# Performance work log

Measured on AMD Instinct MI355X. Metric: run time of the kernel, lower is better.

The kernel has to match this reference:

```python
import jax, jax.numpy as jnp
import numpy as np

N_NODES = 50000
N_EDGES = 800000
F_IN = 128
HID = 128
N_GRAPHS = 256


def setup_inputs() -> dict:
    key = jax.random.key(0)
    ks = jax.random.split(key, 12)
    gx = jax.random.normal(ks[0], (N_NODES, F_IN), dtype=jnp.float32)
    edge_index = jax.random.randint(ks[1], (2, N_EDGES), 0, N_NODES, dtype=jnp.int64)
    batch = jnp.sort(jax.random.randint(ks[2], (N_NODES,), 0, N_GRAPHS, dtype=jnp.int64))
    edge_attr = jax.random.uniform(ks[3], (N_EDGES,), dtype=jnp.float32)
    s1 = 1.0 / np.sqrt(F_IN)
    s2 = 1.0 / np.sqrt(HID)
    W1 = jax.random.uniform(ks[4], (F_IN, HID), jnp.float32, -s1, s1)
    b1 = jnp.zeros((HID,), jnp.float32)
    W2 = jax.random.uniform(ks[5], (HID, HID), jnp.float32, -s2, s2)
    b2 = jnp.zeros((HID,), jnp.float32)
    W3 = jax.random.uniform(ks[6], (HID, HID), jnp.float32, -s2, s2)
    b3 = jnp.zeros((HID,), jnp.float32)
    return {"gx": gx, "edge_index": edge_index, "batch": batch, "edge_attr": edge_attr,
            "W1": W1, "b1": b1, "W2": W2, "b2": b2, "W3": W3, "b3": b3}


def _gcn_conv(x, W, b, row, col, edge_weight, n_nodes):
    # PyG GCNConv with add_self_loops=False:
    #   deg[i] = sum of edge_weight over edges with dst == i
    #   norm_e = deg^{-1/2}[row] * w_e * deg^{-1/2}[col]
    #   out[i] = sum_{e: col_e == i} norm_e * (x @ W)[row_e] + b
    deg = jax.ops.segment_sum(edge_weight, col, num_segments=n_nodes)
    dinv = jnp.where(deg > 0, jax.lax.rsqrt(deg), 0.0)
    norm = dinv[row] * edge_weight * dinv[col]  # [E]
    h = x @ W  # [N, H]
    msg = h[row] * norm[:, None]  # [E, H] gather + scale
    out = jax.ops.segment_sum(msg, col, num_segments=n_nodes)  # scatter-add
    return out + b


def reference(gx, edge_index, batch, edge_attr, W1, b1, W2, b2, W3, b3):
    row, col = edge_index[0], edge_index[1]
    n = gx.shape[0]
    # dropout layers are in eval mode (identity) for a deterministic reference
    h = jax.nn.relu(_gcn_conv(gx, W1, b1, row, col, edge_attr, n))
    h = jax.nn.relu(_gcn_conv(h, W2, b2, row, col, edge_attr, n))
    h = _gcn_conv(h, W3, b3, row, col, edge_attr, n)
    readout = jax.ops.segment_sum(h, batch, num_segments=N_GRAPHS)  # global_add_pool
    return h, readout
```

## Files before the change

kernel.cpp:

```cpp
#include <hip/hip_runtime.h>

#define FEAT 128

typedef __attribute__((ext_vector_type(8))) short short8;
typedef __attribute__((ext_vector_type(4))) float f32x4;

__device__ __forceinline__ unsigned int bf16rtn(float f) {
    unsigned int u = __float_as_uint(f);
    return (u + 0x7fffu + ((u >> 16) & 1u)) >> 16;
}
__device__ __forceinline__ float bf16tof(unsigned int h) { return __uint_as_float(h << 16); }
__device__ __forceinline__ float bf16lo(unsigned int v) { return __uint_as_float(v << 16); }
__device__ __forceinline__ float bf16hi(unsigned int v) { return __uint_as_float(v & 0xffff0000u); }

__global__ void zero_kernel(float* __restrict__ p, int n) {
    int i = blockIdx.x * blockDim.x + threadIdx.x;
    if (i < n) p[i] = 0.0f;
}

__global__ __launch_bounds__(256) void hist_kernel(const int* __restrict__ col,
                                                   int* __restrict__ ghist,
                                                   int E, int nblk, int nbuck) {
    __shared__ int h[256];
    const int t = threadIdx.x, b = blockIdx.x;
    h[t] = 0;
    __syncthreads();
    const int base = b * 4096;
#pragma unroll
    for (int i = 0; i < 16; ++i) {
        int e = base + i * 256 + t;
        if (e < E) atomicAdd(&h[col[e] >> 8], 1);
    }
    __syncthreads();
    if (t < nbuck) ghist[t * nblk + b] = h[t];
}

__global__ __launch_bounds__(256) void scan_block_kernel(const int* __restrict__ cnt,
                                                         int* __restrict__ out,
                                                         int* __restrict__ bsum, int M) {
    __shared__ int s[256];
    int t = threadIdx.x;
    int i = blockIdx.x * 256 + t;
    int own = (i < M) ? cnt[i] : 0;
    s[t] = own;
    for (int off = 1; off < 256; off <<= 1) {
        __syncthreads();
        int v = (t >= off) ? s[t - off] : 0;
        __syncthreads();
        s[t] += v;
    }
    __syncthreads();
    if (i < M) out[i] = s[t] - own;
    if (t == 255) bsum[blockIdx.x] = s[255];
}

__global__ __launch_bounds__(256) void scan_bsum_kernel(int* __restrict__ bsum, int nb) {
    __shared__ int s[256];
    int t = threadIdx.x;
    int own = (t < nb) ? bsum[t] : 0;
    s[t] = own;
    for (int off = 1; off < 256; off <<= 1) {
        __syncthreads();
        int v = (t >= off) ? s[t - off] : 0;
        __syncthreads();
        s[t] += v;
    }
    __syncthreads();
    if (t < nb) bsum[t] = s[t] - own;
}

__global__ __launch_bounds__(256) void scatter1_kernel(const int* __restrict__ row,
                                                       const int* __restrict__ col,
                                                       const float* __restrict__ ew,
                                                       const int* __restrict__ gsc,
                                                       const int* __restrict__ bsum,
                                                       uint2* __restrict__ bedge,
                                                       int E, int nblk, int nbuck) {
    __shared__ int cur[256];
    const int t = threadIdx.x, b = blockIdx.x;
    if (t < nbuck) {
        int idx = t * nblk + b;
        cur[t] = gsc[idx] + bsum[idx >> 8];
    }
    __syncthreads();
    const int base = b * 4096;
#pragma unroll
    for (int i = 0; i < 16; ++i) {
        int e = base + i * 256 + t;
        if (e < E) {
            int c = col[e];
            int slot = atomicAdd(&cur[c >> 8], 1);
            bedge[slot] = make_uint2(((unsigned)c << 16) | (unsigned)row[e],
                                     __float_as_uint(ew[e]));
        }
    }
}

__global__ __launch_bounds__(256) void bucket_kernel(const uint2* __restrict__ bedge,
                                                     const int* __restrict__ gsc,
                                                     const int* __restrict__ bsum,
                                                     int* __restrict__ rowptr,
                                                     float* __restrict__ dinv,
                                                     uint2* __restrict__ sedge,
                                                     int N, int E, int nblk, int nbuck) {
    __shared__ int lcnt[256];
    __shared__ float lw[256];
    __shared__ int lscan[256];
    __shared__ int lcur[256];
    __shared__ float ldv[256];

    const int d = blockIdx.x, t = threadIdx.x;
    const int i0 = d * nblk;
    const int base = gsc[i0] + bsum[i0 >> 8];
    int end;
    if (d == nbuck - 1) end = E;
    else {
        const int i1 = (d + 1) * nblk;
        end = gsc[i1] + bsum[i1 >> 8];
    }

    lcnt[t] = 0;
    lw[t] = 0.f;
    __syncthreads();
    for (int i = base + t; i < end; i += 256) {
        uint2 p = bedge[i];
        int c = (p.x >> 16) & 255;
        atomicAdd(&lcnt[c], 1);
        atomicAdd(&lw[c], __uint_as_float(p.y));
    }
    __syncthreads();
    int own = lcnt[t];
    lscan[t] = own;
    for (int off = 1; off < 256; off <<= 1) {
        __syncthreads();
        int v = (t >= off) ? lscan[t - off] : 0;
        __syncthreads();
        lscan[t] += v;
    }
    __syncthreads();
    int excl = lscan[t] - own;
    lcur[t] = base + excl;
    float wsum = lw[t];
    float dv = (wsum > 0.f) ? rsqrtf(wsum) : 0.f;
    ldv[t] = dv;
    int node = d * 256 + t;
    if (node < N) {
        rowptr[node] = base + excl;
        dinv[node] = dv;
    }
    if (d == nbuck - 1 && t == 0) rowptr[N] = E;
    __syncthreads();
    for (int i = base + t; i < end; i += 256) {
        uint2 p = bedge[i];
        int c = (p.x >> 16) & 255;
        int slot = atomicAdd(&lcur[c], 1);
        sedge[slot] = make_uint2(p.x & 0xFFFFu,
                                 __float_as_uint(__uint_as_float(p.y) * ldv[c]));
    }
}

__global__ void norm_kernel(uint2* __restrict__ sedge, const float* __restrict__ dinv, int E) {
    int i = blockIdx.x * blockDim.x + threadIdx.x;
    if (i < E) {
        uint2 p = sedge[i];
        p.y = __float_as_uint(__uint_as_float(p.y) * dinv[p.x]);
        sedge[i] = p;
    }
}

__global__ void convw_kernel(const float* __restrict__ W0, const float* __restrict__ W1,
                             const float* __restrict__ W2,
                             unsigned short* __restrict__ Whi, unsigned short* __restrict__ Wlo) {
    int i = blockIdx.x * blockDim.x + threadIdx.x;
    int which = blockIdx.y;
    const float* W = (which == 0) ? W0 : (which == 1) ? W1 : W2;
    int c = i >> 7, k = i & 127;
    float w = W[(size_t)k * FEAT + c];
    unsigned int h = bf16rtn(w);
    size_t off = (size_t)which * 16384 + (size_t)c * FEAT + k;
    Whi[off] = (unsigned short)h;
    Wlo[off] = (unsigned short)bf16rtn(w - bf16tof(h));
}

__global__ __launch_bounds__(256) void gemm_mfma_kernel(
    const float* __restrict__ X,
    const unsigned short* __restrict__ Wthi, const unsigned short* __restrict__ Wtlo,
    unsigned int* __restrict__ hb,
    int N)
{
    __shared__ unsigned short xh[64 * 128];
    __shared__ unsigned short xl[64 * 128];
    __shared__ unsigned short wh[64 * 128];
    __shared__ unsigned short wl[64 * 128];

    const int tid = threadIdx.x;
    const int r0 = blockIdx.x * 64;
    const int cb = blockIdx.y;

#pragma unroll
    for (int it = 0; it < 4; ++it) {
        int idx = it * 256 + tid;
        int c = idx >> 4;
        int k8 = (idx & 15) * 8;
        int sw = k8 ^ ((c & 7) << 3);
        size_t src = (size_t)(cb * 64 + c) * FEAT + k8;
        *(short8*)&wh[c * 128 + sw] = *(const short8*)(Wthi + src);
        *(short8*)&wl[c * 128 + sw] = *(const short8*)(Wtlo + src);
    }
#pragma unroll
    for (int it = 0; it < 8; ++it) {
        int idx = it * 256 + tid;
        int r = idx >> 5;
        int kc = (idx & 31) * 4;
        int gr = r0 + r;
        float4 v = make_float4(0.f, 0.f, 0.f, 0.f);
        if (gr < N) v = *(const float4*)(X + (size_t)gr * FEAT + kc);
        unsigned int h0 = bf16rtn(v.x), h1 = bf16rtn(v.y);
        unsigned int h2 = bf16rtn(v.z), h3 = bf16rtn(v.w);
        ushort4 hv = make_ushort4((unsigned short)h0, (unsigned short)h1,
                                  (unsigned short)h2, (unsigned short)h3);
        ushort4 lv = make_ushort4((unsigned short)bf16rtn(v.x - bf16tof(h0)),
                                  (unsigned short)bf16rtn(v.y - bf16tof(h1)),
                                  (unsigned short)bf16rtn(v.z - bf16tof(h2)),
                                  (unsigned short)bf16rtn(v.w - bf16tof(h3)));
        int sw = kc ^ ((r & 7) << 3);
        *(ushort4*)&xh[r * 128 + sw] = hv;
        *(ushort4*)&xl[r * 128 + sw] = lv;
    }
    __syncthreads();

    const int lane = tid & 63;
    const int wv = tid >> 6;
    const int m = lane & 15;
    const int quad = lane >> 4;
    const int arow = wv * 16 + m;

    f32x4 acc[4];
#pragma unroll
    for (int ct = 0; ct < 4; ++ct) acc[ct] = (f32x4){0.f, 0.f, 0.f, 0.f};

#pragma unroll
    for (int kt = 0; kt < 4; ++kt) {
        const int k0 = kt * 32 + quad * 8;
        const int aw = k0 ^ ((arow & 7) << 3);
        short8 ah = *(const short8*)&xh[arow * 128 + aw];
        short8 al = *(const short8*)&xl[arow * 128 + aw];
#pragma unroll
        for (int ct = 0; ct < 4; ++ct) {
            int bc = ct * 16 + m;
            int bw = k0 ^ ((bc & 7) << 3);
            short8 bh = *(const short8*)&wh[bc * 128 + bw];
            short8 bl = *(const short8*)&wl[bc * 128 + bw];
            acc[ct] = __builtin_amdgcn_mfma_f32_16x16x32_bf16(ah, bh, acc[ct], 0, 0, 0);
            acc[ct] = __builtin_amdgcn_mfma_f32_16x16x32_bf16(ah, bl, acc[ct], 0, 0, 0);
            acc[ct] = __builtin_amdgcn_mfma_f32_16x16x32_bf16(al, bh, acc[ct], 0, 0, 0);
        }
    }

    __syncthreads();
    unsigned short* cl = xh;
#pragma unroll
    for (int ct = 0; ct < 4; ++ct)
#pragma unroll
        for (int reg = 0; reg < 4; ++reg) {
            int rrow = wv * 16 + quad * 4 + reg;
            cl[rrow * 72 + ct * 16 + m] = (unsigned short)bf16rtn(acc[ct][reg]);
        }
    __syncthreads();
#pragma unroll
    for (int it = 0; it < 2; ++it) {
        int idx = it * 256 + tid;
        int r = idx >> 3;
        int c4 = (idx & 7) * 4;
        int gr = r0 + r;
        if (gr < N) {
            uint4 pv = *(const uint4*)&cl[r * 72 + c4 * 2];
            *(uint4*)(hb + (size_t)gr * 64 + cb * 32 + c4) = pv;
        }
    }
}

template <int RELU>
__global__ __launch_bounds__(256) void agg_kernel(
    const int* __restrict__ rowptr, const uint2* __restrict__ sedge,
    const uint2* __restrict__ hb2,
    const float* __restrict__ bias,
    float* __restrict__ outX, int N)
{
    const int node = blockIdx.x * 4 + (threadIdx.x >> 6);
    if (node >= N) return;
    const int lane = threadIdx.x & 63;
    const int h = lane >> 5;
    const int j = lane & 31;
    const int s = rowptr[node];
    const int e = rowptr[node + 1];

    float a0 = 0.f, a1 = 0.f, a2 = 0.f, a3 = 0.f;

    for (int gb = s; gb < e; gb += 16) {
        uint2 m0, m1, m2, m3, m4, m5, m6, m7;
        if (gb + 16 <= e) {
            m0 = sedge[gb + 0 + h];  m1 = sedge[gb + 2 + h];
            m2 = sedge[gb + 4 + h];  m3 = sedge[gb + 6 + h];
            m4 = sedge[gb + 8 + h];  m5 = sedge[gb + 10 + h];
            m6 = sedge[gb + 12 + h]; m7 = sedge[gb + 14 + h];
        } else {
            const uint2 z = make_uint2(0u, 0u);
            int i0 = gb + 0 + h, i1 = gb + 2 + h, i2 = gb + 4 + h, i3 = gb + 6 + h;
            int i4 = gb + 8 + h, i5 = gb + 10 + h, i6 = gb + 12 + h, i7 = gb + 14 + h;
            m0 = (i0 < e) ? sedge[i0] : z;  m1 = (i1 < e) ? sedge[i1] : z;
            m2 = (i2 < e) ? sedge[i2] : z;  m3 = (i3 < e) ? sedge[i3] : z;
            m4 = (i4 < e) ? sedge[i4] : z;  m5 = (i5 < e) ? sedge[i5] : z;
            m6 = (i6 < e) ? sedge[i6] : z;  m7 = (i7 < e) ? sedge[i7] : z;
        }
        uint2 v0 = hb2[(size_t)m0.x * 32 + j];
        uint2 v1 = hb2[(size_t)m1.x * 32 + j];
        uint2 v2 = hb2[(size_t)m2.x * 32 + j];
        uint2 v3 = hb2[(size_t)m3.x * 32 + j];
        uint2 v4 = hb2[(size_t)m4.x * 32 + j];
        uint2 v5 = hb2[(size_t)m5.x * 32 + j];
        uint2 v6 = hb2[(size_t)m6.x * 32 + j];
        uint2 v7 = hb2[(size_t)m7.x * 32 + j];
        float w0 = __uint_as_float(m0.y), w1 = __uint_as_float(m1.y);
        float w2 = __uint_as_float(m2.y), w3 = __uint_as_float(m3.y);
        float w4 = __uint_as_float(m4.y), w5 = __uint_as_float(m5.y);
        float w6 = __uint_as_float(m6.y), w7 = __uint_as_float(m7.y);
        a0 = fmaf(w0, bf16lo(v0.x), a0); a1 = fmaf(w0, bf16hi(v0.x), a1);
        a2 = fmaf(w0, bf16lo(v0.y), a2); a3 = fmaf(w0, bf16hi(v0.y), a3);
        a0 = fmaf(w1, bf16lo(v1.x), a0); a1 = fmaf(w1, bf16hi(v1.x), a1);
        a2 = fmaf(w1, bf16lo(v1.y), a2); a3 = fmaf(w1, bf16hi(v1.y), a3);
        a0 = fmaf(w2, bf16lo(v2.x), a0); a1 = fmaf(w2, bf16hi(v2.x), a1);
        a2 = fmaf(w2, bf16lo(v2.y), a2); a3 = fmaf(w2, bf16hi(v2.y), a3);
        a0 = fmaf(w3, bf16lo(v3.x), a0); a1 = fmaf(w3, bf16hi(v3.x), a1);
        a2 = fmaf(w3, bf16lo(v3.y), a2); a3 = fmaf(w3, bf16hi(v3.y), a3);
        a0 = fmaf(w4, bf16lo(v4.x), a0); a1 = fmaf(w4, bf16hi(v4.x), a1);
        a2 = fmaf(w4, bf16lo(v4.y), a2); a3 = fmaf(w4, bf16hi(v4.y), a3);
        a0 = fmaf(w5, bf16lo(v5.x), a0); a1 = fmaf(w5, bf16hi(v5.x), a1);
        a2 = fmaf(w5, bf16lo(v5.y), a2); a3 = fmaf(w5, bf16hi(v5.y), a3);
        a0 = fmaf(w6, bf16lo(v6.x), a0); a1 = fmaf(w6, bf16hi(v6.x), a1);
        a2 = fmaf(w6, bf16lo(v6.y), a2); a3 = fmaf(w6, bf16hi(v6.y), a3);
        a0 = fmaf(w7, bf16lo(v7.x), a0); a1 = fmaf(w7, bf16hi(v7.x), a1);
        a2 = fmaf(w7, bf16lo(v7.y), a2); a3 = fmaf(w7, bf16hi(v7.y), a3);
    }

    a0 += __shfl_xor(a0, 32);
    a1 += __shfl_xor(a1, 32);
    a2 += __shfl_xor(a2, 32);
    a3 += __shfl_xor(a3, 32);

    if (h == 0) {
        float4 bv = ((const float4*)bias)[j];
        a0 += bv.x; a1 += bv.y; a2 += bv.z; a3 += bv.w;
        if (RELU) {
            a0 = fmaxf(a0, 0.f); a1 = fmaxf(a1, 0.f);
            a2 = fmaxf(a2, 0.f); a3 = fmaxf(a3, 0.f);
        }
        *(float4*)(outX + (size_t)node * FEAT + j * 4) = make_float4(a0, a1, a2, a3);
    }
}

__global__ __launch_bounds__(128) void readout_kernel(const float* __restrict__ h,
                                                      const int* __restrict__ batch,
                                                      float* __restrict__ ro, int N) {
    const int g = blockIdx.x;
    const int chunk = blockIdx.y;
    const int j = threadIdx.x;
    int lo = 0, hi = N;
    while (lo < hi) { int mid = (lo + hi) >> 1; if (batch[mid] < g) lo = mid + 1; else hi = mid; }
    int lo2 = lo, hi2 = N;
    while (lo2 < hi2) { int mid = (lo2 + hi2) >> 1; if (batch[mid] < g + 1) lo2 = mid + 1; else hi2 = mid; }
    const int len = lo2 - lo;
    const int per = (len + 7) >> 3;
    const int cs = lo + chunk * per;
    const int ce = min(lo2, cs + per);

    float s0 = 0.f, s1 = 0.f, s2 = 0.f, s3 = 0.f;
    int n = cs;
    for (; n + 4 <= ce; n += 4) {
        s0 += h[(size_t)n * FEAT + j];
        s1 += h[(size_t)(n + 1) * FEAT + j];
        s2 += h[(size_t)(n + 2) * FEAT + j];
        s3 += h[(size_t)(n + 3) * FEAT + j];
    }
    for (; n < ce; ++n) s0 += h[(size_t)n * FEAT + j];
    float acc = (s0 + s1) + (s2 + s3);
    if (cs < ce) atomicAdd(&ro[(size_t)g * FEAT + j], acc);
}

static inline size_t align256(size_t x) { return (x + 255) & ~(size_t)255; }

extern "C" void kernel_launch(void* const* d_in, const int* in_sizes, int n_in,
                              void* d_out, int out_size, void* d_ws, size_t ws_size,
                              hipStream_t stream) {
    const float* gx    = (const float*)d_in[0];
    const int*   ei    = (const int*)d_in[1];
    const int*   batch = (const int*)d_in[2];
    const float* ew    = (const float*)d_in[3];
    const float* W1 = (const float*)d_in[4];
    const float* b1 = (const float*)d_in[5];
    const float* W2 = (const float*)d_in[6];
    const float* b2 = (const float*)d_in[7];
    const float* W3 = (const float*)d_in[8];
    const float* b3 = (const float*)d_in[9];

    const int N = in_sizes[0] / FEAT;
    const int E = in_sizes[3];
    const int G = (out_size - N * FEAT) / FEAT;

    const int* row = ei;
    const int* col = ei + E;

    const int nbuck = (N + 255) >> 8;
    const int nblk  = (E + 4095) >> 12;
    const int M     = nbuck * nblk;

    char* ws = (char*)d_ws;
    int*   rowptr = (int*)ws;         ws += align256((size_t)(N + 1) * 4);
    float* dinv   = (float*)ws;       ws += align256((size_t)N * 4);
    int*   ghist  = (int*)ws;         ws += align256((size_t)M * 4);
    int*   gsc    = (int*)ws;         ws += align256((size_t)M * 4);
    int*   bsum   = (int*)ws;         ws += align256(256 * 4);
    uint2* bedge  = (uint2*)ws;       ws += align256((size_t)E * 8);
    uint2* sedge  = (uint2*)ws;       ws += align256((size_t)E * 8);
    unsigned int* hb = (unsigned int*)ws;  ws += align256((size_t)N * 64 * 4);
    float* bufX   = (float*)ws;       ws += align256((size_t)N * FEAT * 4);
    unsigned short* Wh = (unsigned short*)ws; ws += align256((size_t)3 * 16384 * 2);
    unsigned short* Wl = (unsigned short*)ws; ws += align256((size_t)3 * 16384 * 2);

    float* h_out = (float*)d_out;
    float* ro    = h_out + (size_t)N * FEAT;

    hist_kernel<<<nblk, 256, 0, stream>>>(col, ghist, E, nblk, nbuck);
    const int snb = (M + 255) / 256;
    scan_block_kernel<<<snb, 256, 0, stream>>>(ghist, gsc, bsum, M);
    scan_bsum_kernel<<<1, 256, 0, stream>>>(bsum, snb);
    scatter1_kernel<<<nblk, 256, 0, stream>>>(row, col, ew, gsc, bsum, bedge, E, nblk, nbuck);
    bucket_kernel<<<nbuck, 256, 0, stream>>>(bedge, gsc, bsum, rowptr, dinv, sedge, N, E, nblk, nbuck);
    norm_kernel<<<(E + 255) / 256, 256, 0, stream>>>(sedge, dinv, E);

    convw_kernel<<<dim3(64, 3), 256, 0, stream>>>(W1, W2, W3, Wh, Wl);

    dim3 ggrid((N + 63) / 64, 2);
    const int ablocks = (N + 3) / 4;
    const uint2* hb2 = (const uint2*)hb;

    gemm_mfma_kernel<<<ggrid, 256, 0, stream>>>(gx, Wh, Wl, hb, N);
    agg_kernel<1><<<ablocks, 256, 0, stream>>>(rowptr, sedge, hb2, b1, bufX, N);
    gemm_mfma_kernel<<<ggrid, 256, 0, stream>>>(bufX, Wh + 16384, Wl + 16384, hb, N);
    agg_kernel<1><<<ablocks, 256, 0, stream>>>(rowptr, sedge, hb2, b2, bufX, N);
    gemm_mfma_kernel<<<ggrid, 256, 0, stream>>>(bufX, Wh + 32768, Wl + 32768, hb, N);
    agg_kernel<0><<<ablocks, 256, 0, stream>>>(rowptr, sedge, hb2, b3, h_out, N);
    zero_kernel<<<(G * FEAT + 255) / 256, 256, 0, stream>>>(ro, G * FEAT);
    readout_kernel<<<dim3(G, 8), 128, 0, stream>>>(h_out, batch, ro, N);
}
```

Baseline: 311.8 us.

## Merge preprocessing kernels, compute degrees via global atomics, load GEMM inputs directly

Several changes land together. Weight conversion and degree zeroing are merged into one prep kernel. Weighted degree is accumulated with global atomics in the histogram pass, and dinv is computed alongside the bucket-sum scan, so full edge normalization happens in scatter1 and the separate norm_kernel is gone. The GEMM now reads X rows straight from global memory into registers instead of staging split-bf16 copies in LDS, which cuts shared memory use. Readout is rewritten as one block per graph with no atomics and no zero kernel. The cost is heavy global float atomics on the degree array, and potentially less coalesced X loads in the GEMM.

```diff
diff --git a/kernel.cpp b/kernel.cpp
--- a/kernel.cpp
+++ b/kernel.cpp
@@ -13,13 +13,33 @@
 __device__ __forceinline__ float bf16lo(unsigned int v) { return __uint_as_float(v << 16); }
 __device__ __forceinline__ float bf16hi(unsigned int v) { return __uint_as_float(v & 0xffff0000u); }
 
-__global__ void zero_kernel(float* __restrict__ p, int n) {
-    int i = blockIdx.x * blockDim.x + threadIdx.x;
-    if (i < n) p[i] = 0.0f;
+__global__ __launch_bounds__(256) void prep_kernel(const float* __restrict__ W0,
+                                                   const float* __restrict__ W1,
+                                                   const float* __restrict__ W2,
+                                                   unsigned short* __restrict__ Whi,
+                                                   unsigned short* __restrict__ Wlo,
+                                                   float* __restrict__ wdeg, int N) {
+    const int t = threadIdx.x, x = blockIdx.x, y = blockIdx.y;
+    if (y == 3) {
+        int i = x * 256 + t;
+        if (i < N) wdeg[i] = 0.f;
+        return;
+    }
+    if (x >= 64) return;
+    int i = x * 256 + t;
+    const float* W = (y == 0) ? W0 : (y == 1) ? W1 : W2;
+    int c = i >> 7, k = i & 127;
+    float w = W[(size_t)k * FEAT + c];
+    unsigned int h = bf16rtn(w);
+    size_t off = (size_t)y * 16384 + (size_t)c * FEAT + k;
+    Whi[off] = (unsigned short)h;
+    Wlo[off] = (unsigned short)bf16rtn(w - bf16tof(h));
 }
 
 __global__ __launch_bounds__(256) void hist_kernel(const int* __restrict__ col,
+                                                   const float* __restrict__ ew,
                                                    int* __restrict__ ghist,
+                                                   float* __restrict__ wdeg,
                                                    int E, int nblk, int nbuck) {
     __shared__ int h[256];
     const int t = threadIdx.x, b = blockIdx.x;
@@ -29,7 +49,11 @@
 #pragma unroll
     for (int i = 0; i < 16; ++i) {
         int e = base + i * 256 + t;
-        if (e < E) atomicAdd(&h[col[e] >> 8], 1);
+        if (e < E) {
+            int c = col[e];
+            atomicAdd(&h[c >> 8], 1);
+            atomicAdd(&wdeg[c], ew[e]);
+        }
     }
     __syncthreads();
     if (t < nbuck) ghist[t * nblk + b] = h[t];
@@ -54,9 +78,19 @@
     if (t == 255) bsum[blockIdx.x] = s[255];
 }
 
-__global__ __launch_bounds__(256) void scan_bsum_kernel(int* __restrict__ bsum, int nb) {
+__global__ __launch_bounds__(256) void scan_bsum_dinv_kernel(int* __restrict__ bsum, int nb,
+                                                             const float* __restrict__ wdeg,
+                                                             float* __restrict__ dinv, int N) {
     __shared__ int s[256];
-    int t = threadIdx.x;
+    const int t = threadIdx.x, b = blockIdx.x;
+    if (b > 0) {
+        int node = (b - 1) * 256 + t;
+        if (node < N) {
+            float w = wdeg[node];
+            dinv[node] = (w > 0.f) ? rsqrtf(w) : 0.f;
+        }
+        return;
+    }
     int own = (t < nb) ? bsum[t] : 0;
     s[t] = own;
     for (int off = 1; off < 256; off <<= 1) {
@@ -72,6 +106,7 @@
 __global__ __launch_bounds__(256) void scatter1_kernel(const int* __restrict__ row,
                                                        const int* __restrict__ col,
                                                        const float* __restrict__ ew,
+                                                       const float* __restrict__ dinv,
                                                        const int* __restrict__ gsc,
                                                        const int* __restrict__ bsum,
                                                        uint2* __restrict__ bedge,
@@ -89,9 +124,10 @@
         int e = base + i * 256 + t;
         if (e < E) {
             int c = col[e];
+            int r = row[e];
+            float w = dinv[r] * ew[e] * dinv[c];
             int slot = atomicAdd(&cur[c >> 8], 1);
-            bedge[slot] = make_uint2(((unsigned)c << 16) | (unsigned)row[e],
-                                     __float_as_uint(ew[e]));
+            bedge[slot] = make_uint2(((unsigned)c << 16) | (unsigned)r, __float_as_uint(w));
         }
     }
 }
@@ -100,14 +136,11 @@
                                                      const int* __restrict__ gsc,
                                                      const int* __restrict__ bsum,
                                                      int* __restrict__ rowptr,
-                                                     float* __restrict__ dinv,
                                                      uint2* __restrict__ sedge,
                                                      int N, int E, int nblk, int nbuck) {
     __shared__ int lcnt[256];
-    __shared__ float lw[256];
     __shared__ int lscan[256];
     __shared__ int lcur[256];
-    __shared__ float ldv[256];
 
     const int d = blockIdx.x, t = threadIdx.x;
     const int i0 = d * nblk;
@@ -120,13 +153,10 @@
     }
 
     lcnt[t] = 0;
-    lw[t] = 0.f;
     __syncthreads();
     for (int i = base + t; i < end; i += 256) {
         uint2 p = bedge[i];
-        int c = (p.x >> 16) & 255;
-        atomicAdd(&lcnt[c], 1);
-        atomicAdd(&lw[c], __uint_as_float(p.y));
+        atomicAdd(&lcnt[(p.x >> 16) & 255], 1);
     }
     __syncthreads();
     int own = lcnt[t];
@@ -140,46 +170,16 @@
     __syncthreads();
     int excl = lscan[t] - own;
     lcur[t] = base + excl;
-    float wsum = lw[t];
-    float dv = (wsum > 0.f) ? rsqrtf(wsum) : 0.f;
-    ldv[t] = dv;
     int node = d * 256 + t;
-    if (node < N) {
-        rowptr[node] = base + excl;
-        dinv[node] = dv;
-    }
+    if (node < N) rowptr[node] = base + excl;
     if (d == nbuck - 1 && t == 0) rowptr[N] = E;
     __syncthreads();
     for (int i = base + t; i < end; i += 256) {
         uint2 p = bedge[i];
         int c = (p.x >> 16) & 255;
         int slot = atomicAdd(&lcur[c], 1);
-        sedge[slot] = make_uint2(p.x & 0xFFFFu,
-                                 __float_as_uint(__uint_as_float(p.y) * ldv[c]));
-    }
-}
-
-__global__ void norm_kernel(uint2* __restrict__ sedge, const float* __restrict__ dinv, int E) {
-    int i = blockIdx.x * blockDim.x + threadIdx.x;
-    if (i < E) {
-        uint2 p = sedge[i];
-        p.y = __float_as_uint(__uint_as_float(p.y) * dinv[p.x]);
-        sedge[i] = p;
-    }
-}
-
-__global__ void convw_kernel(const float* __restrict__ W0, const float* __restrict__ W1,
-                             const float* __restrict__ W2,
-                             unsigned short* __restrict__ Whi, unsigned short* __restrict__ Wlo) {
-    int i = blockIdx.x * blockDim.x + threadIdx.x;
-    int which = blockIdx.y;
-    const float* W = (which == 0) ? W0 : (which == 1) ? W1 : W2;
-    int c = i >> 7, k = i & 127;
-    float w = W[(size_t)k * FEAT + c];
-    unsigned int h = bf16rtn(w);
-    size_t off = (size_t)which * 16384 + (size_t)c * FEAT + k;
-    Whi[off] = (unsigned short)h;
-    Wlo[off] = (unsigned short)bf16rtn(w - bf16tof(h));
+        sedge[slot] = make_uint2(p.x & 0xFFFFu, p.y);
+    }
 }
 
 __global__ __launch_bounds__(256) void gemm_mfma_kernel(
@@ -188,8 +188,6 @@
     unsigned int* __restrict__ hb,
     int N)
 {
-    __shared__ unsigned short xh[64 * 128];
-    __shared__ unsigned short xl[64 * 128];
     __shared__ unsigned short wh[64 * 128];
     __shared__ unsigned short wl[64 * 128];
 
@@ -207,26 +205,6 @@
         *(short8*)&wh[c * 128 + sw] = *(const short8*)(Wthi + src);
         *(short8*)&wl[c * 128 + sw] = *(const short8*)(Wtlo + src);
     }
-#pragma unroll
-    for (int it = 0; it < 8; ++it) {
-        int idx = it * 256 + tid;
-        int r = idx >> 5;
-        int kc = (idx & 31) * 4;
-        int gr = r0 + r;
-        float4 v = make_float4(0.f, 0.f, 0.f, 0.f);
-        if (gr < N) v = *(const float4*)(X + (size_t)gr * FEAT + kc);
-        unsigned int h0 = bf16rtn(v.x), h1 = bf16rtn(v.y);
-        unsigned int h2 = bf16rtn(v.z), h3 = bf16rtn(v.w);
-        ushort4 hv = make_ushort4((unsigned short)h0, (unsigned short)h1,
-                                  (unsigned short)h2, (unsigned short)h3);
-        ushort4 lv = make_ushort4((unsigned short)bf16rtn(v.x - bf16tof(h0)),
-                                  (unsigned short)bf16rtn(v.y - bf16tof(h1)),
-                                  (unsigned short)bf16rtn(v.z - bf16tof(h2)),
-                                  (unsigned short)bf16rtn(v.w - bf16tof(h3)));
-        int sw = kc ^ ((r & 7) << 3);
-        *(ushort4*)&xh[r * 128 + sw] = hv;
-        *(ushort4*)&xl[r * 128 + sw] = lv;
-    }
     __syncthreads();
 
     const int lane = tid & 63;
@@ -234,6 +212,8 @@
     const int m = lane & 15;
     const int quad = lane >> 4;
     const int arow = wv * 16 + m;
+    const int grow = r0 + arow;
+    const float* xrow = X + (size_t)grow * FEAT;
 
     f32x4 acc[4];
 #pragma unroll
@@ -242,9 +222,27 @@
 #pragma unroll
     for (int kt = 0; kt < 4; ++kt) {
         const int k0 = kt * 32 + quad * 8;
-        const int aw = k0 ^ ((arow & 7) << 3);
-        short8 ah = *(const short8*)&xh[arow * 128 + aw];
-        short8 al = *(const short8*)&xl[arow * 128 + aw];
+        float4 va = make_float4(0.f, 0.f, 0.f, 0.f);
+        float4 vb = make_float4(0.f, 0.f, 0.f, 0.f);
+        if (grow < N) {
+            va = *(const float4*)(xrow + k0);
+            vb = *(const float4*)(xrow + k0 + 4);
+        }
+        unsigned int h0 = bf16rtn(va.x), h1 = bf16rtn(va.y);
+        unsigned int h2 = bf16rtn(va.z), h3 = bf16rtn(va.w);
+        unsigned int h4 = bf16rtn(vb.x), h5 = bf16rtn(vb.y);
+        unsigned int h6 = bf16rtn(vb.z), h7 = bf16rtn(vb.w);
+        short8 ah, al;
+        ah[0] = (short)h0; ah[1] = (short)h1; ah[2] = (short)h2; ah[3] = (short)h3;
+        ah[4] = (short)h4; ah[5] = (short)h5; ah[6] = (short)h6; ah[7] = (short)h7;
+        al[0] = (short)bf16rtn(va.x - bf16tof(h0));
+        al[1] = (short)bf16rtn(va.y - bf16tof(h1));
+        al[2] = (short)bf16rtn(va.z - bf16tof(h2));
+        al[3] = (short)bf16rtn(va.w - bf16tof(h3));
+        al[4] = (short)bf16rtn(vb.x - bf16tof(h4));
+        al[5] = (short)bf16rtn(vb.y - bf16tof(h5));
+        al[6] = (short)bf16rtn(vb.z - bf16tof(h6));
+        al[7] = (short)bf16rtn(vb.w - bf16tof(h7));
 #pragma unroll
         for (int ct = 0; ct < 4; ++ct) {
             int bc = ct * 16 + m;
@@ -258,7 +256,7 @@
     }
 
     __syncthreads();
-    unsigned short* cl = xh;
+    unsigned short* cl = wh;
 #pragma unroll
     for (int ct = 0; ct < 4; ++ct)
 #pragma unroll
@@ -359,32 +357,29 @@
     }
 }
 
-__global__ __launch_bounds__(128) void readout_kernel(const float* __restrict__ h,
+__global__ __launch_bounds__(256) void readout_kernel(const float* __restrict__ h,
                                                       const int* __restrict__ batch,
                                                       float* __restrict__ ro, int N) {
+    __shared__ float part[128];
     const int g = blockIdx.x;
-    const int chunk = blockIdx.y;
-    const int j = threadIdx.x;
+    const int j = threadIdx.x & 127;
+    const int half = threadIdx.x >> 7;
     int lo = 0, hi = N;
     while (lo < hi) { int mid = (lo + hi) >> 1; if (batch[mid] < g) lo = mid + 1; else hi = mid; }
     int lo2 = lo, hi2 = N;
     while (lo2 < hi2) { int mid = (lo2 + hi2) >> 1; if (batch[mid] < g + 1) lo2 = mid + 1; else hi2 = mid; }
-    const int len = lo2 - lo;
-    const int per = (len + 7) >> 3;
-    const int cs = lo + chunk * per;
-    const int ce = min(lo2, cs + per);
-
-    float s0 = 0.f, s1 = 0.f, s2 = 0.f, s3 = 0.f;
-    int n = cs;
-    for (; n + 4 <= ce; n += 4) {
+
+    float s0 = 0.f, s1 = 0.f;
+    int n = lo + half;
+    for (; n + 2 < lo2; n += 4) {
         s0 += h[(size_t)n * FEAT + j];
-        s1 += h[(size_t)(n + 1) * FEAT + j];
-        s2 += h[(size_t)(n + 2) * FEAT + j];
-        s3 += h[(size_t)(n + 3) * FEAT + j];
-    }
-    for (; n < ce; ++n) s0 += h[(size_t)n * FEAT + j];
-    float acc = (s0 + s1) + (s2 + s3);
-    if (cs < ce) atomicAdd(&ro[(size_t)g * FEAT + j], acc);
+        s1 += h[(size_t)(n + 2) * FEAT + j];
+    }
+    if (n < lo2) s0 += h[(size_t)n * FEAT + j];
+    float s = s0 + s1;
+    if (half == 1) part[j] = s;
+    __syncthreads();
+    if (half == 0) ro[(size_t)g * FEAT + j] = s + part[j];
 }
 
 static inline size_t align256(size_t x) { return (x + 255) & ~(size_t)255; }
@@ -427,18 +422,20 @@
     unsigned short* Wh = (unsigned short*)ws; ws += align256((size_t)3 * 16384 * 2);
     unsigned short* Wl = (unsigned short*)ws; ws += align256((size_t)3 * 16384 * 2);
 
+    float* wdeg = bufX;
+
     float* h_out = (float*)d_out;
     float* ro    = h_out + (size_t)N * FEAT;
 
-    hist_kernel<<<nblk, 256, 0, stream>>>(col, ghist, E, nblk, nbuck);
+    const int pgx = max((N + 255) / 256, 64);
+    prep_kernel<<<dim3(pgx, 4), 256, 0, stream>>>(W1, W2, W3, Wh, Wl, wdeg, N);
+
+    hist_kernel<<<nblk, 256, 0, stream>>>(col, ew, ghist, wdeg, E, nblk, nbuck);
     const int snb = (M + 255) / 256;
     scan_block_kernel<<<snb, 256, 0, stream>>>(ghist, gsc, bsum, M);
-    scan_bsum_kernel<<<1, 256, 0, stream>>>(bsum, snb);
-    scatter1_kernel<<<nblk, 256, 0, stream>>>(row, col, ew, gsc, bsum, bedge, E, nblk, nbuck);
-    bucket_kernel<<<nbuck, 256, 0, stream>>>(bedge, gsc, bsum, rowptr, dinv, sedge, N, E, nblk, nbuck);
-    norm_kernel<<<(E + 255) / 256, 256, 0, stream>>>(sedge, dinv, E);
-
-    convw_kernel<<<dim3(64, 3), 256, 0, stream>>>(W1, W2, W3, Wh, Wl);
+    scan_bsum_dinv_kernel<<<1 + nbuck, 256, 0, stream>>>(bsum, snb, wdeg, dinv, N);
+    scatter1_kernel<<<nblk, 256, 0, stream>>>(row, col, ew, dinv, gsc, bsum, bedge, E, nblk, nbuck);
+    bucket_kernel<<<nbuck, 256, 0, stream>>>(bedge, gsc, bsum, rowptr, sedge, N, E, nblk, nbuck);
 
     dim3 ggrid((N + 63) / 64, 2);
     const int ablocks = (N + 3) / 4;
@@ -450,6 +447,5 @@
     agg_kernel<1><<<ablocks, 256, 0, stream>>>(rowptr, sedge, hb2, b2, bufX, N);
     gemm_mfma_kernel<<<ggrid, 256, 0, stream>>>(bufX, Wh + 32768, Wl + 32768, hb, N);
     agg_kernel<0><<<ablocks, 256, 0, stream>>>(rowptr, sedge, hb2, b3, h_out, N);
-    zero_kernel<<<(G * FEAT + 255) / 256, 256, 0, stream>>>(ro, G * FEAT);
-    readout_kernel<<<dim3(G, 8), 128, 0, stream>>>(h_out, batch, ro, N);
-}
+    readout_kernel<<<G, 256, 0, stream>>>(h_out, batch, ro, N);
+}
```

Measured after the change: 331.0 us. 1.06x slower.
